# Performance work log

Measured on AMD Instinct MI355X. Metric: run time of the kernel, lower is better.

Reference implementation:

```python
import jax, jax.numpy as jnp
import numpy as np

N_NODES = 5
B, C, H, W = 4, 256, 32, 32
THRESH = 0.3
EPS = 1e-12


def setup_inputs() -> dict:
    key = jax.random.key(0)
    k1, k2, k3, k4 = jax.random.split(key, 4)
    x = jax.random.normal(k1, (N_NODES, B, C, H, W), dtype=jnp.float32)
    w = jax.random.normal(k2, (N_NODES, N_NODES), dtype=jnp.float32)
    # 5 stacked conv1x1 'experts': Conv2d(2C -> C, k=1) weight [C,2C] + bias [C]
    conv_w = jax.random.normal(k3, (N_NODES, C, 2 * C), dtype=jnp.float32) * 0.02
    conv_b = jax.random.normal(k4, (N_NODES, C), dtype=jnp.float32) * 0.02
    return {"x": x, "w": w, "conv_w": conv_w, "conv_b": conv_b}


def reference(x, w, conv_w, conv_b):
    # x: [N, B, C, H, W] -- the list of N node feature maps stacked
    N, b, c, h, ww = x.shape
    P = b * c * h * ww  # 'pixels' = total element count of one node tensor

    # conv_i(cat(node_j, node_i + node_j)) splits into W1@node_j + W2@(node_i+node_j) + b_i
    W1 = conv_w[:, :, :c]          # [N, C, C] acts on node_j
    W2 = conv_w[:, :, c:]          # [N, C, C] acts on node_i + node_j
    A = W1 + W2                    # combined weight on node_j

    term_j = jnp.einsum('ick,jbkhw->ijbchw', A, x)    # [N,N,B,C,H,W]
    term_i = jnp.einsum('ick,ibkhw->ibchw', W2, x)    # [N,B,C,H,W]
    target = term_j + term_i[:, None] + conv_b[:, None, None, :, None, None]
    distance = x[None, :] - target                    # distance[i,j] = node_j - conv_i(...)

    # edge_list[:, i, j] = flatten(distance[i, j])  -> [P, N, N]
    edge = distance.reshape(N, N, P).transpose(2, 0, 1)

    # new_edge = edge * w; sigmoid; threshold at 0.3; L2-normalize over dim=2 (j axis)
    e = jax.nn.sigmoid(edge * w)
    e = jnp.where(e > THRESH, e, jnp.zeros_like(e))
    norm = jnp.sqrt(jnp.sum(e * e, axis=2, keepdims=True))
    e = e / jnp.maximum(norm, EPS)

    # node matrix: [P, N] of flattened node features; fuse h[p,i] = sum_j e[p,i,j]*node[p,j]
    node = x.reshape(N, P).T
    hmat = jnp.einsum('pij,pj->pi', e, node)          # [P, N]
    return hmat.T.reshape(N, b, c, h, ww)
```

## Files before the change

### kernel.cpp

```cpp
#include <hip/hip_runtime.h>
#include <cmath>

#define NN  5
#define BB  4
#define CCH 256
#define HWD 1024
#define THRESH_V 0.3f
#define EPS_V 1e-12f


#define CT 64
#define WT 64
#define KC 32
#define APAD 68
#define SPAD 68

#define W2T_OFF (NN * CCH * CCH)

#define AS_FLOATS   (KC * APAD)
#define ES_FLOATS   (6 * 16 * SPAD)
#define SMEM_FLOATS ES_FLOATS

__global__ void fub_prep(const float* __restrict__ conv_w, float* __restrict__ ws)
{
    const int t = blockIdx.x * 256 + threadIdx.x;
    if (t >= NN * CCH * 64) return;
    const int c4 = (t & 63) << 2;
    const int k  = (t >> 6) & 255;
    const int i  = t >> 14;
    float s1[4], s2[4];
#pragma unroll
    for (int cc = 0; cc < 4; ++cc) {
        const float* p = conv_w + (size_t)(i * CCH + c4 + cc) * (2 * CCH) + k;
        const float w1 = p[0];
        const float w2 = p[CCH];
        s1[cc] = w1 + w2;
        s2[cc] = w2;
    }
    float* At  = ws + (size_t)(i * CCH + k) * CCH + c4;
    float* W2t = ws + W2T_OFF + (size_t)(i * CCH + k) * CCH + c4;
    *(float4*)At  = make_float4(s1[0], s1[1], s1[2], s1[3]);
    *(float4*)W2t = make_float4(s2[0], s2[1], s2[2], s2[3]);
}

__global__ __launch_bounds__(384, 3)
void fub_main(const float* __restrict__ x, const float* __restrict__ wmat,
              const float* __restrict__ ws, const float* __restrict__ conv_b,
              float* __restrict__ out)
{
    __shared__ __align__(16) float smem[SMEM_FLOATS];
    float* As  = smem;
    float* W2s = smem + AS_FLOATS;
    float* Es  = smem;

    const int tid  = threadIdx.x;
    const int wv   = tid >> 6;
    const int lane = tid & 63;

    const int wg  = blockIdx.x;
    int L = (wg & 7) * 160 + (wg >> 3);
    const int i   = L % 5;  L /= 5;
    const int ct  = L & 3;  L >>= 2;
    const int b   = L & 3;  L >>= 2;
    const int hwt = L;

    const int c0  = ct * CT;
    const int hw0 = hwt * WT;

    const int lr = (lane >> 3) << 3;
    const int lc = (lane & 7)  << 3;

    const int jx = (wv < NN) ? wv : i;
    const float* Ms = (wv == 5) ? W2s : As;
    const float* Mb = Ms + lr;
    const float* xrow = x + (size_t)((jx * BB + b) * CCH) * HWD + hw0 + lc;

    float acc[8][8];
#pragma unroll
    for (int r = 0; r < 8; ++r)
#pragma unroll
        for (int c = 0; c < 8; ++c) acc[r][c] = 0.0f;

    float4 xn0 = *(const float4*)(xrow);
    float4 xn1 = *(const float4*)(xrow + 4);

    for (int k0 = 0; k0 < CCH; k0 += KC) {
#pragma unroll
        for (int it = 0; it < 3; ++it) {
            const int idx = tid + it * 384;
            if (idx < 1024) {
                const int tbl = idx >> 9;
                const int rem = idx & 511;
                const int kk  = rem >> 4;
                const int c4  = (rem & 15) << 2;
                const float4 v = *(const float4*)(
                    ws + (size_t)(tbl ? W2T_OFF : 0)
                       + (size_t)(i * CCH + k0 + kk) * CCH + c0 + c4);
                *(float4*)((tbl ? W2s : As) + kk * APAD + c4) = v;
            }
        }
        __syncthreads();

#pragma unroll 4
        for (int kk = 0; kk < KC; ++kk) {
            const float4 xc0 = xn0, xc1 = xn1;
            const int kn = (k0 + kk + 1) & 255;
            xn0 = *(const float4*)(xrow + (size_t)kn * HWD);
            xn1 = *(const float4*)(xrow + (size_t)kn * HWD + 4);

            const float4 a0 = *(const float4*)(Mb + kk * APAD);
            const float4 a1 = *(const float4*)(Mb + kk * APAD + 4);
            const float ar[8] = {a0.x, a0.y, a0.z, a0.w, a1.x, a1.y, a1.z, a1.w};
            const float xv[8] = {xc0.x, xc0.y, xc0.z, xc0.w, xc1.x, xc1.y, xc1.z, xc1.w};
#pragma unroll
            for (int r = 0; r < 8; ++r)
#pragma unroll
                for (int c = 0; c < 8; ++c)
                    acc[r][c] = fmaf(ar[r], xv[c], acc[r][c]);
        }
        __syncthreads();
    }

    const int rhme  = lr >> 4;
    const int rbase = lr & 15;

    float wrow[NN];
#pragma unroll
    for (int j = 0; j < NN; ++j) wrow[j] = wmat[i * NN + j];

#pragma unroll
    for (int rh = 0; rh < 4; ++rh) {
        if (rhme == rh) {
            float* Eb = Es + wv * (16 * SPAD) + lc;
#pragma unroll
            for (int r = 0; r < 8; ++r) {
                *(float4*)(Eb + (rbase + r) * SPAD) =
                    make_float4(acc[r][0], acc[r][1], acc[r][2], acc[r][3]);
                *(float4*)(Eb + (rbase + r) * SPAD + 4) =
                    make_float4(acc[r][4], acc[r][5], acc[r][6], acc[r][7]);
            }
        }
        __syncthreads();

        if (tid < 256) {
            const int row  = tid >> 4;
            const int colq = (tid & 15) << 2;
            const int c    = c0 + rh * 16 + row;
            const float bias = conv_b[i * CCH + c];

            const float4 T = *(const float4*)(Es + 5 * (16 * SPAD) + row * SPAD + colq);
            const float Tv[4] = {T.x, T.y, T.z, T.w};

            float num[4] = {0.f, 0.f, 0.f, 0.f};
            float sq [4] = {0.f, 0.f, 0.f, 0.f};
#pragma unroll
            for (int j = 0; j < NN; ++j) {
                const float4 s  = *(const float4*)(Es + j * (16 * SPAD) + row * SPAD + colq);
                const float4 xj = *(const float4*)(
                    x + (size_t)((j * BB + b) * CCH + c) * HWD + hw0 + colq);
                const float sv[4] = {s.x, s.y, s.z, s.w};
                const float xv[4] = {xj.x, xj.y, xj.z, xj.w};
#pragma unroll
                for (int cc = 0; cc < 4; ++cc) {
                    const float target = sv[cc] + Tv[cc] + bias;
                    const float dist   = xv[cc] - target;
                    const float z      = dist * wrow[j];
                    float e = 1.0f / (1.0f + expf(-z));
                    e = (e > THRESH_V) ? e : 0.0f;
                    sq[cc]  = fmaf(e, e, sq[cc]);
                    num[cc] = fmaf(e, xv[cc], num[cc]);
                }
            }
            float4 res;
            res.x = num[0] / fmaxf(sqrtf(sq[0]), EPS_V);
            res.y = num[1] / fmaxf(sqrtf(sq[1]), EPS_V);
            res.z = num[2] / fmaxf(sqrtf(sq[2]), EPS_V);
            res.w = num[3] / fmaxf(sqrtf(sq[3]), EPS_V);
            *(float4*)(out + (size_t)((i * BB + b) * CCH + c) * HWD + hw0 + colq) = res;
        }
        __syncthreads();
    }
}

extern "C" void kernel_launch(void* const* d_in, const int* in_sizes, int n_in,
                              void* d_out, int out_size, void* d_ws, size_t ws_size,
                              hipStream_t stream) {
    const float* x      = (const float*)d_in[0];
    const float* w      = (const float*)d_in[1];
    const float* conv_w = (const float*)d_in[2];
    const float* conv_b = (const float*)d_in[3];
    float* out = (float*)d_out;
    float* ws  = (float*)d_ws;

    fub_prep<<<dim3(320), dim3(256), 0, stream>>>(conv_w, ws);

    fub_main<<<dim3(1280), dim3(384), 0, stream>>>(x, w, ws, conv_b, out);
}
```

Baseline: 329.3 us.

## Stage x tiles in shared memory instead of per-lane global register prefetch

Each k-chunk now loads the x tile for all five nodes into LDS, using 256 threads for x and 128 threads for the weight tiles. The inner loop reads x from shared memory instead of issuing global loads with a one-step register prefetch. KC is halved to 16 so the larger shared buffer still fits. This is meant to remove redundant and poorly coalesced global x loads, since the W2 wave reloads node i's data. The cost is twice as many barrier rounds, no overlap between loads and compute, and more LDS traffic.

New measurement: 328.1 us. No clear change (-0.4%).

```diff
diff --git a/kernel.cpp b/kernel.cpp
--- a/kernel.cpp
+++ b/kernel.cpp
@@ -11,15 +11,16 @@
 
 #define CT 64
 #define WT 64
-#define KC 32
+#define KC 16
 #define APAD 68
 #define SPAD 68
 
 #define W2T_OFF (NN * CCH * CCH)
 
-#define AS_FLOATS   (KC * APAD)
-#define ES_FLOATS   (6 * 16 * SPAD)
-#define SMEM_FLOATS ES_FLOATS
+#define XS_FLOATS (NN * KC * WT)
+#define AS_OFF    XS_FLOATS
+#define W2S_OFF   (AS_OFF + KC * APAD)
+#define SMEM_FLOATS (W2S_OFF + KC * APAD)
 
 __global__ void fub_prep(const float* __restrict__ conv_w, float* __restrict__ ws)
 {
@@ -49,8 +50,9 @@
               float* __restrict__ out)
 {
     __shared__ __align__(16) float smem[SMEM_FLOATS];
-    float* As  = smem;
-    float* W2s = smem + AS_FLOATS;
+    float* Xs  = smem;
+    float* As  = smem + AS_OFF;
+    float* W2s = smem + W2S_OFF;
     float* Es  = smem;
 
     const int tid  = threadIdx.x;
@@ -73,7 +75,7 @@
     const int jx = (wv < NN) ? wv : i;
     const float* Ms = (wv == 5) ? W2s : As;
     const float* Mb = Ms + lr;
-    const float* xrow = x + (size_t)((jx * BB + b) * CCH) * HWD + hw0 + lc;
+    const float* Xb = Xs + jx * (KC * WT) + lc;
 
     float acc[8][8];
 #pragma unroll
@@ -81,16 +83,26 @@
 #pragma unroll
         for (int c = 0; c < 8; ++c) acc[r][c] = 0.0f;
 
-    float4 xn0 = *(const float4*)(xrow);
-    float4 xn1 = *(const float4*)(xrow + 4);
-
     for (int k0 = 0; k0 < CCH; k0 += KC) {
-#pragma unroll
-        for (int it = 0; it < 3; ++it) {
-            const int idx = tid + it * 384;
-            if (idx < 1024) {
-                const int tbl = idx >> 9;
-                const int rem = idx & 511;
+        if (tid < 256) {
+#pragma unroll
+            for (int it = 0; it < 5; ++it) {
+                const int t   = tid + it * 256;
+                const int j   = t >> 8;
+                const int rem = t & 255;
+                const int kk  = rem >> 4;
+                const int q4  = (rem & 15) << 2;
+                const float4 v = *(const float4*)(
+                    x + (size_t)((j * BB + b) * CCH + k0 + kk) * HWD + hw0 + q4);
+                *(float4*)(Xs + j * (KC * WT) + kk * WT + q4) = v;
+            }
+        } else {
+            const int u = tid - 256;
+#pragma unroll
+            for (int it = 0; it < 4; ++it) {
+                const int t   = u + it * 128;
+                const int tbl = t >> 8;
+                const int rem = t & 255;
                 const int kk  = rem >> 4;
                 const int c4  = (rem & 15) << 2;
                 const float4 v = *(const float4*)(
@@ -103,20 +115,17 @@
 
 #pragma unroll 4
         for (int kk = 0; kk < KC; ++kk) {
-            const float4 xc0 = xn0, xc1 = xn1;
-            const int kn = (k0 + kk + 1) & 255;
-            xn0 = *(const float4*)(xrow + (size_t)kn * HWD);
-            xn1 = *(const float4*)(xrow + (size_t)kn * HWD + 4);
-
             const float4 a0 = *(const float4*)(Mb + kk * APAD);
             const float4 a1 = *(const float4*)(Mb + kk * APAD + 4);
+            const float4 x0 = *(const float4*)(Xb + kk * WT);
+            const float4 x1 = *(const float4*)(Xb + kk * WT + 4);
             const float ar[8] = {a0.x, a0.y, a0.z, a0.w, a1.x, a1.y, a1.z, a1.w};
-            const float xv[8] = {xc0.x, xc0.y, xc0.z, xc0.w, xc1.x, xc1.y, xc1.z, xc1.w};
+            const float xc[8] = {x0.x, x0.y, x0.z, x0.w, x1.x, x1.y, x1.z, x1.w};
 #pragma unroll
             for (int r = 0; r < 8; ++r)
 #pragma unroll
                 for (int c = 0; c < 8; ++c)
-                    acc[r][c] = fmaf(ar[r], xv[c], acc[r][c]);
+                    acc[r][c] = fmaf(ar[r], xc[c], acc[r][c]);
         }
         __syncthreads();
     }
```

## Stage x tiles through double-buffered LDS with split loader roles

Applied to the files above, without the earlier changes.

The per-lane global loads of x inside the inner k loop are replaced by cooperative staging of x tiles for all five nodes into shared memory, alongside the weight tiles. Two LDS buffers are used so the next K chunk (now 16) is loaded while the current one is computed. Threads 0-255 load x and threads 256-383 load the weights. This removes redundant global x reads across lanes and gives better overlap of loads with compute, at the cost of larger LDS use (about 57KB), which may lower occupancy, and the loss of padding, which may cause bank conflicts.

Result: slower. 358.7 us (+8.9%).

```diff
diff --git a/kernel.cpp b/kernel.cpp
--- a/kernel.cpp
+++ b/kernel.cpp
@@ -11,15 +11,15 @@
 
 #define CT 64
 #define WT 64
-#define KC 32
-#define APAD 68
+#define KC 16
 #define SPAD 68
 
 #define W2T_OFF (NN * CCH * CCH)
 
-#define AS_FLOATS   (KC * APAD)
-#define ES_FLOATS   (6 * 16 * SPAD)
-#define SMEM_FLOATS ES_FLOATS
+#define BUFSZ   7168
+#define AS_OFF  5120
+#define W2S_OFF 6144
+#define SMEM_FLOATS (2 * BUFSZ)
 
 __global__ void fub_prep(const float* __restrict__ conv_w, float* __restrict__ ws)
 {
@@ -43,15 +43,13 @@
     *(float4*)W2t = make_float4(s2[0], s2[1], s2[2], s2[3]);
 }
 
-__global__ __launch_bounds__(384, 3)
+__global__ __launch_bounds__(384) __attribute__((amdgpu_waves_per_eu(2, 3)))
 void fub_main(const float* __restrict__ x, const float* __restrict__ wmat,
               const float* __restrict__ ws, const float* __restrict__ conv_b,
               float* __restrict__ out)
 {
     __shared__ __align__(16) float smem[SMEM_FLOATS];
-    float* As  = smem;
-    float* W2s = smem + AS_FLOATS;
-    float* Es  = smem;
+    float* Es = smem;
 
     const int tid  = threadIdx.x;
     const int wv   = tid >> 6;
@@ -70,10 +68,57 @@
     const int lr = (lane >> 3) << 3;
     const int lc = (lane & 7)  << 3;
 
-    const int jx = (wv < NN) ? wv : i;
-    const float* Ms = (wv == 5) ? W2s : As;
-    const float* Mb = Ms + lr;
-    const float* xrow = x + (size_t)((jx * BB + b) * CCH) * HWD + hw0 + lc;
+    const int jx    = (wv < NN) ? wv : i;
+    const int msoff = (wv == 5) ? W2S_OFF : AS_OFF;
+    const float* Mb = smem + msoff + lr;
+    const float* Xb = smem + jx * (KC * WT) + lc;
+
+    const bool xrole = (tid < 256);
+    const float *p0, *p1, *p2, *p3, *p4;
+    int l0, l1, l2, l3, l4;
+    if (xrole) {
+#define XSET(IT, P, LV) { const int idx = tid + IT * 256;               \
+        const int j = idx >> 8, rem = idx & 255;                        \
+        const int kk = rem >> 4, q4 = (rem & 15) << 2;                  \
+        P  = x + (size_t)((j * BB + b) * CCH + kk) * HWD + hw0 + q4;    \
+        LV = j * (KC * WT) + kk * 64 + q4; }
+        XSET(0, p0, l0) XSET(1, p1, l1) XSET(2, p2, l2) XSET(3, p3, l3) XSET(4, p4, l4)
+#undef XSET
+    } else {
+        const int u = tid - 256;
+#define ASET(IT, P, LV) { const int idx = u + IT * 128;                 \
+        const int tbl = idx >> 8, rem = idx & 255;                      \
+        const int kk = rem >> 4, c4 = (rem & 15) << 2;                  \
+        P  = ws + (size_t)(tbl ? W2T_OFF : 0)                           \
+               + (size_t)(i * CCH + kk) * CCH + c0 + c4;                \
+        LV = (tbl ? W2S_OFF : AS_OFF) + kk * 64 + c4; }
+        ASET(0, p0, l0) ASET(1, p1, l1) ASET(2, p2, l2) ASET(3, p3, l3)
+#undef ASET
+        p4 = p3; l4 = l3;
+    }
+
+    float4 s0, s1, s2, s3, s4;
+
+#define STAGE_LOAD() do {                                               \
+        s0 = *(const float4*)p0; s1 = *(const float4*)p1;               \
+        s2 = *(const float4*)p2; s3 = *(const float4*)p3;               \
+        if (xrole) {                                                    \
+            s4 = *(const float4*)p4;                                    \
+            p0 += KC * HWD; p1 += KC * HWD; p2 += KC * HWD;             \
+            p3 += KC * HWD; p4 += KC * HWD;                             \
+        } else {                                                        \
+            p0 += KC * CCH; p1 += KC * CCH;                             \
+            p2 += KC * CCH; p3 += KC * CCH;                             \
+        }                                                               \
+    } while (0)
+
+#define STAGE_WRITE(BO) do {                                            \
+        *(float4*)(smem + (BO) + l0) = s0;                              \
+        *(float4*)(smem + (BO) + l1) = s1;                              \
+        *(float4*)(smem + (BO) + l2) = s2;                              \
+        *(float4*)(smem + (BO) + l3) = s3;                              \
+        if (xrole) *(float4*)(smem + (BO) + l4) = s4;                   \
+    } while (0)
 
     float acc[8][8];
 #pragma unroll
@@ -81,43 +126,36 @@
 #pragma unroll
         for (int c = 0; c < 8; ++c) acc[r][c] = 0.0f;
 
-    float4 xn0 = *(const float4*)(xrow);
-    float4 xn1 = *(const float4*)(xrow + 4);
-
-    for (int k0 = 0; k0 < CCH; k0 += KC) {
-#pragma unroll
-        for (int it = 0; it < 3; ++it) {
-            const int idx = tid + it * 384;
-            if (idx < 1024) {
-                const int tbl = idx >> 9;
-                const int rem = idx & 511;
-                const int kk  = rem >> 4;
-                const int c4  = (rem & 15) << 2;
-                const float4 v = *(const float4*)(
-                    ws + (size_t)(tbl ? W2T_OFF : 0)
-                       + (size_t)(i * CCH + k0 + kk) * CCH + c0 + c4);
-                *(float4*)((tbl ? W2s : As) + kk * APAD + c4) = v;
-            }
-        }
-        __syncthreads();
-
-#pragma unroll 4
-        for (int kk = 0; kk < KC; ++kk) {
-            const float4 xc0 = xn0, xc1 = xn1;
-            const int kn = (k0 + kk + 1) & 255;
-            xn0 = *(const float4*)(xrow + (size_t)kn * HWD);
-            xn1 = *(const float4*)(xrow + (size_t)kn * HWD + 4);
-
-            const float4 a0 = *(const float4*)(Mb + kk * APAD);
-            const float4 a1 = *(const float4*)(Mb + kk * APAD + 4);
-            const float ar[8] = {a0.x, a0.y, a0.z, a0.w, a1.x, a1.y, a1.z, a1.w};
-            const float xv[8] = {xc0.x, xc0.y, xc0.z, xc0.w, xc1.x, xc1.y, xc1.z, xc1.w};
-#pragma unroll
-            for (int r = 0; r < 8; ++r)
-#pragma unroll
-                for (int c = 0; c < 8; ++c)
-                    acc[r][c] = fmaf(ar[r], xv[c], acc[r][c]);
-        }
+#define COMPUTE(BO) do {                                                \
+        _Pragma("unroll 4")                                             \
+        for (int kk = 0; kk < KC; ++kk) {                               \
+            const float4 a0 = *(const float4*)(Mb + (BO) + kk * 64);    \
+            const float4 a1 = *(const float4*)(Mb + (BO) + kk * 64 + 4);\
+            const float4 x0 = *(const float4*)(Xb + (BO) + kk * 64);    \
+            const float4 x1 = *(const float4*)(Xb + (BO) + kk * 64 + 4);\
+            const float ar[8] = {a0.x,a0.y,a0.z,a0.w,a1.x,a1.y,a1.z,a1.w}; \
+            const float xc[8] = {x0.x,x0.y,x0.z,x0.w,x1.x,x1.y,x1.z,x1.w}; \
+            _Pragma("unroll")                                           \
+            for (int r = 0; r < 8; ++r)                                 \
+                _Pragma("unroll")                                       \
+                for (int c = 0; c < 8; ++c)                             \
+                    acc[r][c] = fmaf(ar[r], xc[c], acc[r][c]);          \
+        }                                                               \
+    } while (0)
+
+    STAGE_LOAD();
+    STAGE_WRITE(0);
+    __syncthreads();
+
+#pragma unroll 1
+    for (int t = 0; t < 8; ++t) {
+        STAGE_LOAD();
+        COMPUTE(0);
+        STAGE_WRITE(BUFSZ);
+        __syncthreads();
+        if (t < 7) STAGE_LOAD();
+        COMPUTE(BUFSZ);
+        if (t < 7) STAGE_WRITE(0);
         __syncthreads();
     }
 
```

## Double-buffer x and weight tiles in LDS via async global_load_lds

Applied to the files above, without the earlier changes.

The main GEMM loop now stages both x and the A/W2 weight slices into double-buffered LDS using the global_load_lds direct-to-LDS path with KC=8, so the next chunk loads while the current one computes. Previously x was register-prefetched straight from global memory and the weights went through registers into LDS. The prep kernel now transposes through LDS tiles with coalesced reads and writes and launches fewer blocks. The intent is to hide global latency and cut register and VMEM pressure, at the cost of more barriers, a swizzled layout and a larger LDS footprint.

After: 844.2 us. 2.56x slower.

```diff
diff --git a/kernel.cpp b/kernel.cpp
--- a/kernel.cpp
+++ b/kernel.cpp
@@ -11,36 +11,58 @@
 
 #define CT 64
 #define WT 64
-#define KC 32
-#define APAD 68
+#define KC 8
 #define SPAD 68
 
 #define W2T_OFF (NN * CCH * CCH)
 
-#define AS_FLOATS   (KC * APAD)
-#define ES_FLOATS   (6 * 16 * SPAD)
-#define SMEM_FLOATS ES_FLOATS
+#define BUFSZ 3584
+#define ASO   2560
+#define W2SO  3072
+#define SMEM_FLOATS (2 * BUFSZ)
+
+#define GL16(GSRC, LDST)                                                    \
+    __builtin_amdgcn_global_load_lds(                                       \
+        (const __attribute__((address_space(1))) unsigned int*)(GSRC),      \
+        (__attribute__((address_space(3))) unsigned int*)(LDST), 16, 0, 0)
 
 __global__ void fub_prep(const float* __restrict__ conv_w, float* __restrict__ ws)
 {
-    const int t = blockIdx.x * 256 + threadIdx.x;
-    if (t >= NN * CCH * 64) return;
-    const int c4 = (t & 63) << 2;
-    const int k  = (t >> 6) & 255;
-    const int i  = t >> 14;
-    float s1[4], s2[4];
-#pragma unroll
-    for (int cc = 0; cc < 4; ++cc) {
-        const float* p = conv_w + (size_t)(i * CCH + c4 + cc) * (2 * CCH) + k;
-        const float w1 = p[0];
-        const float w2 = p[CCH];
-        s1[cc] = w1 + w2;
-        s2[cc] = w2;
-    }
-    float* At  = ws + (size_t)(i * CCH + k) * CCH + c4;
-    float* W2t = ws + W2T_OFF + (size_t)(i * CCH + k) * CCH + c4;
-    *(float4*)At  = make_float4(s1[0], s1[1], s1[2], s1[3]);
-    *(float4*)W2t = make_float4(s2[0], s2[1], s2[2], s2[3]);
+    __shared__ float Ta[64 * 68];
+    __shared__ float Tw[64 * 68];
+    const int u  = threadIdx.x;
+    int bid = blockIdx.x;
+    const int cb = bid & 3;  bid >>= 2;
+    const int kb = bid & 3;  bid >>= 2;
+    const int i  = bid;
+
+#pragma unroll
+    for (int p = 0; p < 4; ++p) {
+        const int cl = p * 16 + (u >> 4);
+        const int kq = (u & 15) << 2;
+        const float* g = conv_w + (size_t)(i * CCH + cb * 64 + cl) * (2 * CCH)
+                       + kb * 64 + kq;
+        const float4 w1 = *(const float4*)g;
+        const float4 w2 = *(const float4*)(g + CCH);
+        *(float4*)(Ta + cl * 68 + kq) =
+            make_float4(w1.x + w2.x, w1.y + w2.y, w1.z + w2.z, w1.w + w2.w);
+        *(float4*)(Tw + cl * 68 + kq) = w2;
+    }
+    __syncthreads();
+
+#pragma unroll
+    for (int p = 0; p < 4; ++p) {
+        const int kl = p * 16 + (u >> 4);
+        const int cq = (u & 15) << 2;
+        float4 va, vw;
+        va.x = Ta[(cq + 0) * 68 + kl];  vw.x = Tw[(cq + 0) * 68 + kl];
+        va.y = Ta[(cq + 1) * 68 + kl];  vw.y = Tw[(cq + 1) * 68 + kl];
+        va.z = Ta[(cq + 2) * 68 + kl];  vw.z = Tw[(cq + 2) * 68 + kl];
+        va.w = Ta[(cq + 3) * 68 + kl];  vw.w = Tw[(cq + 3) * 68 + kl];
+        float* o = ws + (size_t)(i * CCH + kb * 64 + kl) * CCH + cb * 64 + cq;
+        *(float4*)o = va;
+        *(float4*)(o + W2T_OFF) = vw;
+    }
 }
 
 __global__ __launch_bounds__(384, 3)
@@ -49,9 +71,7 @@
               float* __restrict__ out)
 {
     __shared__ __align__(16) float smem[SMEM_FLOATS];
-    float* As  = smem;
-    float* W2s = smem + AS_FLOATS;
-    float* Es  = smem;
+    float* Es = smem;
 
     const int tid  = threadIdx.x;
     const int wv   = tid >> 6;
@@ -67,60 +87,71 @@
     const int c0  = ct * CT;
     const int hw0 = hwt * WT;
 
+    const int q    = lane & 15;
+    const int invc = ((q & 7) << 1) | (q >> 3);
+    const int kr   = lane >> 4;
+
+    const int jst = (wv < NN) ? wv : 0;
+    const float* xsrc = x + ((size_t)(jst * BB + b) * CCH + kr) * HWD
+                          + hw0 + invc * 4;
+    const float* asrc  = ws + ((size_t)(i * CCH) + kr) * CCH + c0 + invc * 4;
+    const float* w2src = asrc + W2T_OFF;
+
+    const int jx    = (wv < NN) ? wv : i;
+    const int msoff = (wv == 5) ? W2SO : ASO;
+    const int aoff  = msoff + ((lane >> 3) << 2);
+    const int xoff  = jx * 512 + ((lane & 7) << 2);
+
+    float acc[8][8];
+#pragma unroll
+    for (int r = 0; r < 8; ++r)
+#pragma unroll
+        for (int c = 0; c < 8; ++c) acc[r][c] = 0.0f;
+
+#define STAGE(K0, BO) do {                                                  \
+        if (wv < NN) {                                                      \
+            GL16(xsrc + (size_t)(K0) * HWD,           smem + (BO) + wv * 512);       \
+            GL16(xsrc + (size_t)(K0) * HWD + 4 * HWD, smem + (BO) + wv * 512 + 256); \
+        } else {                                                            \
+            GL16(asrc  + (K0) * CCH,           smem + (BO) + ASO);          \
+            GL16(asrc  + (K0) * CCH + 4 * CCH, smem + (BO) + ASO + 256);    \
+            GL16(w2src + (K0) * CCH,           smem + (BO) + W2SO);         \
+            GL16(w2src + (K0) * CCH + 4 * CCH, smem + (BO) + W2SO + 256);   \
+        }                                                                   \
+    } while (0)
+
+#define COMPUTE(BO) do {                                                    \
+        _Pragma("unroll")                                                   \
+        for (int kk = 0; kk < KC; ++kk) {                                   \
+            const float4 a0 = *(const float4*)(smem + (BO) + aoff + kk * 64);      \
+            const float4 a1 = *(const float4*)(smem + (BO) + aoff + kk * 64 + 32); \
+            const float4 x0 = *(const float4*)(smem + (BO) + xoff + kk * 64);      \
+            const float4 x1 = *(const float4*)(smem + (BO) + xoff + kk * 64 + 32); \
+            const float ar[8] = {a0.x,a0.y,a0.z,a0.w,a1.x,a1.y,a1.z,a1.w};  \
+            const float xc[8] = {x0.x,x0.y,x0.z,x0.w,x1.x,x1.y,x1.z,x1.w};  \
+            _Pragma("unroll")                                               \
+            for (int r = 0; r < 8; ++r)                                     \
+                _Pragma("unroll")                                           \
+                for (int c = 0; c < 8; ++c)                                 \
+                    acc[r][c] = fmaf(ar[r], xc[c], acc[r][c]);              \
+        }                                                                   \
+    } while (0)
+
+    STAGE(0, 0);
+    __syncthreads();
+
+#pragma unroll 1
+    for (int t = 0; t < 32; t += 2) {
+        STAGE((t + 1) * KC, BUFSZ);
+        COMPUTE(0);
+        __syncthreads();
+        if (t < 30) STAGE((t + 2) * KC, 0);
+        COMPUTE(BUFSZ);
+        __syncthreads();
+    }
+
     const int lr = (lane >> 3) << 3;
     const int lc = (lane & 7)  << 3;
-
-    const int jx = (wv < NN) ? wv : i;
-    const float* Ms = (wv == 5) ? W2s : As;
-    const float* Mb = Ms + lr;
-    const float* xrow = x + (size_t)((jx * BB + b) * CCH) * HWD + hw0 + lc;
-
-    float acc[8][8];
-#pragma unroll
-    for (int r = 0; r < 8; ++r)
-#pragma unroll
-        for (int c = 0; c < 8; ++c) acc[r][c] = 0.0f;
-
-    float4 xn0 = *(const float4*)(xrow);
-    float4 xn1 = *(const float4*)(xrow + 4);
-
-    for (int k0 = 0; k0 < CCH; k0 += KC) {
-#pragma unroll
-        for (int it = 0; it < 3; ++it) {
-            const int idx = tid + it * 384;
-            if (idx < 1024) {
-                const int tbl = idx >> 9;
-                const int rem = idx & 511;
-                const int kk  = rem >> 4;
-                const int c4  = (rem & 15) << 2;
-                const float4 v = *(const float4*)(
-                    ws + (size_t)(tbl ? W2T_OFF : 0)
-                       + (size_t)(i * CCH + k0 + kk) * CCH + c0 + c4);
-                *(float4*)((tbl ? W2s : As) + kk * APAD + c4) = v;
-            }
-        }
-        __syncthreads();
-
-#pragma unroll 4
-        for (int kk = 0; kk < KC; ++kk) {
-            const float4 xc0 = xn0, xc1 = xn1;
-            const int kn = (k0 + kk + 1) & 255;
-            xn0 = *(const float4*)(xrow + (size_t)kn * HWD);
-            xn1 = *(const float4*)(xrow + (size_t)kn * HWD + 4);
-
-            const float4 a0 = *(const float4*)(Mb + kk * APAD);
-            const float4 a1 = *(const float4*)(Mb + kk * APAD + 4);
-            const float ar[8] = {a0.x, a0.y, a0.z, a0.w, a1.x, a1.y, a1.z, a1.w};
-            const float xv[8] = {xc0.x, xc0.y, xc0.z, xc0.w, xc1.x, xc1.y, xc1.z, xc1.w};
-#pragma unroll
-            for (int r = 0; r < 8; ++r)
-#pragma unroll
-                for (int c = 0; c < 8; ++c)
-                    acc[r][c] = fmaf(ar[r], xv[c], acc[r][c]);
-        }
-        __syncthreads();
-    }
-
     const int rhme  = lr >> 4;
     const int rbase = lr & 15;
 
@@ -192,7 +223,7 @@
     float* out = (float*)d_out;
     float* ws  = (float*)d_ws;
 
-    fub_prep<<<dim3(320), dim3(256), 0, stream>>>(conv_w, ws);
+    fub_prep<<<dim3(80), dim3(256), 0, stream>>>(conv_w, ws);
 
     fub_main<<<dim3(1280), dim3(384), 0, stream>>>(x, w, ws, conv_b, out);
 }
```
